# Optimization experiments

Hardware: AMD Instinct MI355X
Metric: run time of the kernel (lower is better)

The kernel has to match this reference:

```python
import jax, jax.numpy as jnp
import numpy as np

B, N, D, S, ITERS, EPS = 32, 4096, 512, 8, 3, 1e-8


def layer_norm(x, g, b, eps=1e-5):
    mu = jnp.mean(x, axis=-1, keepdims=True)
    var = jnp.var(x, axis=-1, keepdims=True)
    return (x - mu) * jax.lax.rsqrt(var + eps) * g + b


def setup_inputs() -> dict:
    key = jax.random.key(0)
    ks = jax.random.split(key, 12)
    sc = 1.0 / np.sqrt(D)
    return {
        "inputs": jax.random.normal(ks[0], (B, N, D), jnp.float32),
        "noise": jax.random.normal(ks[1], (B, S, D), jnp.float32),
        "slots_mu": jax.random.normal(ks[2], (1, S, D), jnp.float32),
        "slots_sigma": jnp.ones((1, S, D), jnp.float32),
        "ln_in_g": jnp.ones((D,), jnp.float32), "ln_in_b": jnp.zeros((D,), jnp.float32),
        "ln_s_g": jnp.ones((D,), jnp.float32), "ln_s_b": jnp.zeros((D,), jnp.float32),
        "wq": jax.random.normal(ks[3], (D, D), jnp.float32) * sc,
        "wk": jax.random.normal(ks[4], (D, D), jnp.float32) * sc,
        "wv": jax.random.normal(ks[5], (D, D), jnp.float32) * sc,
        "w_ih": jax.random.normal(ks[6], (3 * D, D), jnp.float32) * sc,
        "w_hh": jax.random.normal(ks[7], (3 * D, D), jnp.float32) * sc,
        "b_ih": jnp.zeros((3 * D,), jnp.float32),
        "b_hh": jnp.zeros((3 * D,), jnp.float32),
        "ln_m_g": jnp.ones((D,), jnp.float32), "ln_m_b": jnp.zeros((D,), jnp.float32),
        "w1": jax.random.normal(ks[8], (D, D), jnp.float32) * sc,
        "b1": jnp.zeros((D,), jnp.float32),
        "w2": jax.random.normal(ks[9], (D, D), jnp.float32) * sc,
        "b2": jnp.zeros((D,), jnp.float32),
    }


def reference(inputs, noise, slots_mu, slots_sigma, ln_in_g, ln_in_b, ln_s_g, ln_s_b,
              wq, wk, wv, w_ih, w_hh, b_ih, b_hh, ln_m_g, ln_m_b, w1, b1, w2, b2):
    # slot init: mu + sigma * N(0,1)
    slots = slots_mu + slots_sigma * noise          # (B,S,D)
    x = layer_norm(inputs, ln_in_g, ln_in_b)        # (B,N,D)
    k = jnp.einsum('bnd,ed->bne', x, wk)            # (B,N,D)
    v = jnp.einsum('bnd,ed->bne', x, wv)            # (B,N,D)
    for _ in range(ITERS):
        slots_prev = slots
        sn = layer_norm(slots, ln_s_g, ln_s_b)
        q = jnp.einsum('bsd,ed->bse', sn, wq)       # (B,S,D)
        logits = jnp.einsum('bnd,bsd->bns', k, q)   # (B,N,S)
        attn = jax.nn.softmax(logits, axis=-1) + EPS  # softmax over slots
        attn = attn / jnp.sum(attn, axis=-1, keepdims=True)
        attn_t = jnp.swapaxes(attn, -1, -2)         # (B,S,N)
        updates = jnp.einsum('bsn,bnd->bsd', attn_t, v)
        # GRUCell(input=updates, hidden=slots_prev)
        gi = jnp.einsum('bsd,ed->bse', updates, w_ih) + b_ih
        gh = jnp.einsum('bsd,ed->bse', slots_prev, w_hh) + b_hh
        gi_r, gi_z, gi_n = jnp.split(gi, 3, axis=-1)
        gh_r, gh_z, gh_n = jnp.split(gh, 3, axis=-1)
        r = jax.nn.sigmoid(gi_r + gh_r)
        z = jax.nn.sigmoid(gi_z + gh_z)
        n = jnp.tanh(gi_n + r * gh_n)
        slots = (1.0 - z) * n + z * slots_prev
        # residual MLP
        h = layer_norm(slots, ln_m_g, ln_m_b)
        h = jax.nn.relu(jnp.einsum('bsd,ed->bse', h, w1) + b1)
        slots = slots + jnp.einsum('bsd,ed->bse', h, w2) + b2
    return slots
```

## Files before the change

kernel.cpp:

```cpp
#include <hip/hip_runtime.h>

#define B_ 32
#define N_ 4096
#define D_ 512
#define S_ 8
#define ITERS_ 3

__device__ __forceinline__ float sigmoid_f(float x) {
    return 1.0f / (1.0f + __expf(-x));
}
__device__ __forceinline__ float tanh_f(float x) {
    float e = __expf(2.0f * x);
    return 1.0f - 2.0f / (e + 1.0f);
}

__global__ __launch_bounds__(256) void k_init(const float* __restrict__ noise,
                                              const float* __restrict__ mu,
                                              const float* __restrict__ sg,
                                              float* __restrict__ slots,
                                              float* __restrict__ stats) {
    int wid = threadIdx.x >> 6, lane = threadIdx.x & 63;
    int row = blockIdx.x * 4 + wid;
    const float4* nz = (const float4*)(noise + (size_t)row * D_);
    const float4* m4 = (const float4*)(mu + (size_t)(row & 7) * D_);
    const float4* s4 = (const float4*)(sg + (size_t)(row & 7) * D_);
    float4 v0 = nz[lane], v1 = nz[64 + lane];
    float4 a0 = m4[lane], a1 = m4[64 + lane];
    float4 c0 = s4[lane], c1 = s4[64 + lane];
    v0.x = fmaf(c0.x, v0.x, a0.x); v0.y = fmaf(c0.y, v0.y, a0.y);
    v0.z = fmaf(c0.z, v0.z, a0.z); v0.w = fmaf(c0.w, v0.w, a0.w);
    v1.x = fmaf(c1.x, v1.x, a1.x); v1.y = fmaf(c1.y, v1.y, a1.y);
    v1.z = fmaf(c1.z, v1.z, a1.z); v1.w = fmaf(c1.w, v1.w, a1.w);
    float4* o4 = (float4*)(slots + (size_t)row * D_);
    o4[lane] = v0; o4[64 + lane] = v1;
    float s1 = v0.x + v0.y + v0.z + v0.w + v1.x + v1.y + v1.z + v1.w;
    float s2 = v0.x*v0.x; s2 = fmaf(v0.y,v0.y,s2); s2 = fmaf(v0.z,v0.z,s2); s2 = fmaf(v0.w,v0.w,s2);
    s2 = fmaf(v1.x,v1.x,s2); s2 = fmaf(v1.y,v1.y,s2); s2 = fmaf(v1.z,v1.z,s2); s2 = fmaf(v1.w,v1.w,s2);
#pragma unroll
    for (int off = 32; off > 0; off >>= 1) {
        s1 += __shfl_xor(s1, off, 64);
        s2 += __shfl_xor(s2, off, 64);
    }
    if (lane == 0) {
        float mean = s1 * (1.0f / D_);
        float var  = s2 * (1.0f / D_) - mean * mean;
        stats[row * 2]     = mean;
        stats[row * 2 + 1] = rsqrtf(var + 1e-5f);
    }
}

template<int WT, int LNA>
__global__ __launch_bounds__(256) void k_gemm(const float* __restrict__ A,
                                              const float* __restrict__ W,
                                              const float* __restrict__ bias,
                                              float* __restrict__ C,
                                              int M, int N, int K,
                                              const float* __restrict__ stats,
                                              const float* __restrict__ lng,
                                              const float* __restrict__ lnb) {
    __shared__ float As[64][68];
    __shared__ float Ws[64][36];
    int t  = threadIdx.x;
    int bm = blockIdx.y * 64, bn = blockIdx.x * 32;
    int tm = t >> 4, tn = t & 15;
    float acc[4][2] = {{0.f,0.f},{0.f,0.f},{0.f,0.f},{0.f,0.f}};

    for (int kk = 0; kk < K; kk += 64) {
        __syncthreads();
        if (WT == 2) {
#pragma unroll
            for (int r = 0; r < 4; ++r) {
                int idx = t + r * 256;
                int k = idx >> 4, m4 = idx & 15;
                float4 a4 = *(const float4*)(A + (size_t)(kk + k) * M + bm + (m4 << 2));
                *(float4*)&As[k][m4 << 2] = a4;
            }
        } else {
#pragma unroll
            for (int r = 0; r < 4; ++r) {
                int flat = t * 4 + r * 1024;
                int m = flat >> 6, k = flat & 63;
                float4 a4 = *(const float4*)(A + (size_t)(bm + m) * K + kk + k);
                if (LNA) {
                    float mean = stats[(bm + m) * 2];
                    float rs   = stats[(bm + m) * 2 + 1];
                    float4 g4 = *(const float4*)(lng + kk + k);
                    float4 b4 = *(const float4*)(lnb + kk + k);
                    a4.x = fmaf((a4.x - mean) * rs, g4.x, b4.x);
                    a4.y = fmaf((a4.y - mean) * rs, g4.y, b4.y);
                    a4.z = fmaf((a4.z - mean) * rs, g4.z, b4.z);
                    a4.w = fmaf((a4.w - mean) * rs, g4.w, b4.w);
                }
                As[k + 0][m] = a4.x; As[k + 1][m] = a4.y;
                As[k + 2][m] = a4.z; As[k + 3][m] = a4.w;
            }
        }
        if (WT == 1) {
#pragma unroll
            for (int r = 0; r < 2; ++r) {
                int flat = t * 4 + r * 1024;
                int n = flat >> 6, k = flat & 63;
                float4 w4 = *(const float4*)(W + (size_t)(bn + n) * K + kk + k);
                Ws[k + 0][n] = w4.x; Ws[k + 1][n] = w4.y;
                Ws[k + 2][n] = w4.z; Ws[k + 3][n] = w4.w;
            }
        } else {
#pragma unroll
            for (int r = 0; r < 2; ++r) {
                int flat = t * 4 + r * 1024;
                int k = flat >> 5, n = flat & 31;
                float4 w4 = *(const float4*)(W + (size_t)(kk + k) * N + bn + n);
                *(float4*)&Ws[k][n] = w4;
            }
        }
        __syncthreads();
#pragma unroll
        for (int k = 0; k < 64; ++k) {
            float4 a = *(const float4*)&As[k][tm << 2];
            float2 w = *(const float2*)&Ws[k][tn << 1];
            acc[0][0] = fmaf(a.x, w.x, acc[0][0]); acc[0][1] = fmaf(a.x, w.y, acc[0][1]);
            acc[1][0] = fmaf(a.y, w.x, acc[1][0]); acc[1][1] = fmaf(a.y, w.y, acc[1][1]);
            acc[2][0] = fmaf(a.z, w.x, acc[2][0]); acc[2][1] = fmaf(a.z, w.y, acc[2][1]);
            acc[3][0] = fmaf(a.w, w.x, acc[3][0]); acc[3][1] = fmaf(a.w, w.y, acc[3][1]);
        }
    }
#pragma unroll
    for (int i = 0; i < 4; ++i) {
#pragma unroll
        for (int j = 0; j < 2; ++j) {
            int row = bm + (tm << 2) + i;
            int col = bn + (tn << 1) + j;
            float v = acc[i][j];
            if (bias) v += bias[col];
            C[(size_t)row * N + col] = v;
        }
    }
}

__global__ __launch_bounds__(512, 2) void k_attn3(const float* __restrict__ x,
                                                  const float* __restrict__ qk,
                                                  const float* __restrict__ g,
                                                  const float* __restrict__ bvec,
                                                  float* __restrict__ part,
                                                  float* __restrict__ bsum) {
    __shared__ float qts[4096];
    __shared__ float u0s[4096];
    __shared__ float red[64];
    __shared__ float red2[64];
    __shared__ float c12[16];
    const int nc = blockIdx.x, b = blockIdx.y;
    const int t = threadIdx.x;
    const int w = t >> 6, lane = t & 63;

    {
        const float4* qk4 = (const float4*)(qk + (size_t)b * 4096);
        const float4* g4 = (const float4*)g;
        const float4* b4 = (const float4*)bvec;
        float c1p[2], c2p[2];
#pragma unroll
        for (int r = 0; r < 2; ++r) {
            int f = t + r * 512;
            float4 v = qk4[f];
            float4 gg = g4[f & 127];
            float4 bb = b4[f & 127];
            float4 qv = make_float4(v.x*gg.x, v.y*gg.y, v.z*gg.z, v.w*gg.w);
            *(float4*)&qts[((f & 127) * 8 + (f >> 7)) * 4] = qv;
            c1p[r] = qv.x + qv.y + qv.z + qv.w;
            c2p[r] = bb.x*v.x + bb.y*v.y + bb.z*v.z + bb.w*v.w;
        }
#pragma unroll
        for (int off = 32; off > 0; off >>= 1) {
#pragma unroll
            for (int r = 0; r < 2; ++r) {
                c1p[r] += __shfl_xor(c1p[r], off, 64);
                c2p[r] += __shfl_xor(c2p[r], off, 64);
            }
        }
        if (lane == 0) {
            red[w * 2 + 0] = c1p[0]; red[w * 2 + 1] = c1p[1];
            red2[w * 2 + 0] = c2p[0]; red2[w * 2 + 1] = c2p[1];
        }
    }
    __syncthreads();
    if (t < 8) {
        int s = t;
        float v1, v2;
        if (s < 4) { v1 = red[4*s]       + red[4*s + 2];       v2 = red2[4*s]       + red2[4*s + 2]; }
        else       { v1 = red[4*(s-4)+1] + red[4*(s-4)+3];     v2 = red2[4*(s-4)+1] + red2[4*(s-4)+3]; }
        c12[s] = v1; c12[8 + s] = v2;
    }
    __syncthreads();

    float4 qa[8], qb[8];
#pragma unroll
    for (int s = 0; s < 8; ++s) {
        qa[s] = *(const float4*)&qts[(lane * 8 + s) * 4];
        qb[s] = *(const float4*)&qts[((64 + lane) * 8 + s) * 4];
    }
    const int gq = (lane >> 3) & 7;
    const float c1g = c12[gq], c2g = c12[8 + gq];
    const bool hb5 = (lane & 32) != 0, hb4 = (lane & 16) != 0, hb3 = (lane & 8) != 0;
    const int gbase = lane & 7;
    const float cnorm = 1.0f / (1.0f + 8.0f * 1e-8f);
    const float eadd  = 1e-8f * cnorm;

    float4 acc0[8], acc1[8];
#pragma unroll
    for (int s = 0; s < 8; ++s) {
        acc0[s] = make_float4(0.f, 0.f, 0.f, 0.f);
        acc1[s] = make_float4(0.f, 0.f, 0.f, 0.f);
    }
    float aS = 0.f, tS = 0.f;

    const float4* xr = (const float4*)(x + ((size_t)b * N_ + (size_t)nc * 256 + w * 32) * D_);
    float4 xa0 = xr[lane],        xb0 = xr[64 + lane];
    float4 xa1 = xr[128 + lane],  xb1 = xr[192 + lane];

    for (int j = 0; j < 32; ++j) {
        int jn = (j < 30) ? j + 2 : 31;
        float4 na = xr[jn * 128 + lane], nb = xr[jn * 128 + 64 + lane];

        float sx = xa0.x + xa0.y + xa0.z + xa0.w + xb0.x + xb0.y + xb0.z + xb0.w;
        float sxx = xa0.x*xa0.x; sxx = fmaf(xa0.y,xa0.y,sxx); sxx = fmaf(xa0.z,xa0.z,sxx); sxx = fmaf(xa0.w,xa0.w,sxx);
        sxx = fmaf(xb0.x,xb0.x,sxx); sxx = fmaf(xb0.y,xb0.y,sxx); sxx = fmaf(xb0.z,xb0.z,sxx); sxx = fmaf(xb0.w,xb0.w,sxx);
        float dd[8];
#pragma unroll
        for (int s = 0; s < 8; ++s) {
            float td = xa0.x * qa[s].x;
            td = fmaf(xa0.y, qa[s].y, td); td = fmaf(xa0.z, qa[s].z, td); td = fmaf(xa0.w, qa[s].w, td);
            td = fmaf(xb0.x, qb[s].x, td); td = fmaf(xb0.y, qb[s].y, td);
            td = fmaf(xb0.z, qb[s].z, td); td = fmaf(xb0.w, qb[s].w, td);
            dd[s] = td;
        }
        float r4[4];
#pragma unroll
        for (int s = 0; s < 4; ++s) {
            float snd = hb5 ? dd[s] : dd[s + 4];
            float kp  = hb5 ? dd[s + 4] : dd[s];
            r4[s] = kp + __shfl_xor(snd, 32, 64);
        }
        float r2[2];
#pragma unroll
        for (int s = 0; s < 2; ++s) {
            float snd = hb4 ? r4[s] : r4[s + 2];
            float kp  = hb4 ? r4[s + 2] : r4[s];
            r2[s] = kp + __shfl_xor(snd, 16, 64);
        }
        float v;
        {
            float snd = hb3 ? r2[0] : r2[1];
            float kp  = hb3 ? r2[1] : r2[0];
            v = kp + __shfl_xor(snd, 8, 64);
        }
        v += __shfl_xor(v, 4, 64);
        v += __shfl_xor(v, 2, 64);
        v += __shfl_xor(v, 1, 64);
#pragma unroll
        for (int off = 32; off > 0; off >>= 1) {
            sx  += __shfl_xor(sx, off, 64);
            sxx += __shfl_xor(sxx, off, 64);
        }
        float mean = sx * (1.0f / D_);
        float rs   = rsqrtf(sxx * (1.0f / D_) - mean * mean + 1e-5f);
        float lg   = fmaf(rs, v, fmaf(-rs * mean, c1g, c2g));
        float mx = lg;
        mx = fmaxf(mx, __shfl_xor(mx, 8, 64));
        mx = fmaxf(mx, __shfl_xor(mx, 16, 64));
        mx = fmaxf(mx, __shfl_xor(mx, 32, 64));
        float p = __expf(lg - mx);
        float ps = p;
        ps += __shfl_xor(ps, 8, 64);
        ps += __shfl_xor(ps, 16, 64);
        ps += __shfl_xor(ps, 32, 64);
        float a  = fmaf(p, cnorm / ps, eadd);
        float wv = a * rs;
        aS += a;
        tS = fmaf(wv, mean, tS);
        float w8[8];
#pragma unroll
        for (int s = 0; s < 8; ++s) w8[s] = __shfl(wv, (s << 3) | gbase, 64);
#pragma unroll
        for (int s = 0; s < 8; ++s) {
            acc0[s].x = fmaf(w8[s], xa0.x, acc0[s].x); acc0[s].y = fmaf(w8[s], xa0.y, acc0[s].y);
            acc0[s].z = fmaf(w8[s], xa0.z, acc0[s].z); acc0[s].w = fmaf(w8[s], xa0.w, acc0[s].w);
            acc1[s].x = fmaf(w8[s], xb0.x, acc1[s].x); acc1[s].y = fmaf(w8[s], xb0.y, acc1[s].y);
            acc1[s].z = fmaf(w8[s], xb0.z, acc1[s].z); acc1[s].w = fmaf(w8[s], xb0.w, acc1[s].w);
        }
        xa0 = xa1; xb0 = xb1; xa1 = na; xb1 = nb;
    }

    if ((lane & 7) == 0) { red[w * 8 + gq] = aS; red2[w * 8 + gq] = tS; }
    for (int w2 = 0; w2 < 8; ++w2) {
        if (w == w2) {
#pragma unroll
            for (int s = 0; s < 8; ++s) {
                float* p0 = &u0s[s * 512 + (lane << 2)];
                float* p1 = p0 + 256;
                if (w2 == 0) {
                    *(float4*)p0 = acc0[s];
                    *(float4*)p1 = acc1[s];
                } else {
                    float4 v0 = *(float4*)p0;
                    v0.x += acc0[s].x; v0.y += acc0[s].y; v0.z += acc0[s].z; v0.w += acc0[s].w;
                    *(float4*)p0 = v0;
                    float4 v1 = *(float4*)p1;
                    v1.x += acc1[s].x; v1.y += acc1[s].y; v1.z += acc1[s].z; v1.w += acc1[s].w;
                    *(float4*)p1 = v1;
                }
            }
        }
        __syncthreads();
    }
    if (t < 16) {
        int s = t & 7;
        const float* src = (t < 8) ? red : red2;
        float v = 0.f;
#pragma unroll
        for (int w2 = 0; w2 < 8; ++w2) v += src[w2 * 8 + s];
        bsum[(size_t)(b * 16 + nc) * 16 + t] = v;
    }
    float4* d4 = (float4*)(part + (size_t)(b * 16 + nc) * 4096);
    const float4* s4 = (const float4*)u0s;
    d4[t] = s4[t];
    d4[t + 512] = s4[t + 512];
}

__global__ __launch_bounds__(256) void k_ured(const float* __restrict__ part,
                                              const float* __restrict__ bsum,
                                              const float* __restrict__ g,
                                              const float* __restrict__ bvec,
                                              float* __restrict__ u0) {
    __shared__ float avs[16];
    const int b = blockIdx.x, t = threadIdx.x;
    if (t < 16) {
        float v = 0.f;
#pragma unroll
        for (int nc = 0; nc < 16; ++nc) v += bsum[(size_t)(b * 16 + nc) * 16 + t];
        avs[t] = v;
    }
    __syncthreads();
    const int d0 = t * 2;
    float gg0 = g[d0], gg1 = g[d0 + 1], bb0 = bvec[d0], bb1 = bvec[d0 + 1];
#pragma unroll
    for (int s = 0; s < 8; ++s) {
        float p0 = 0.f, p1 = 0.f;
#pragma unroll
        for (int nc = 0; nc < 16; ++nc) {
            float2 pv = *(const float2*)(part + (size_t)(b * 16 + nc) * 4096 + s * 512 + d0);
            p0 += pv.x; p1 += pv.y;
        }
        float Av = avs[s], Tv = avs[8 + s];
        float* o = u0 + (size_t)(b * 8 + s) * D_ + d0;
        o[0] = fmaf(gg0, p0 - Tv, Av * bb0);
        o[1] = fmaf(gg1, p1 - Tv, Av * bb1);
    }
}

__global__ __launch_bounds__(256) void k_gg(const float* __restrict__ slots,
                                            const float* __restrict__ u0,
                                            const float* __restrict__ w_hh,
                                            const float* __restrict__ Wiv,
                                            const float* __restrict__ b_hh,
                                            const float* __restrict__ b_ih,
                                            float* __restrict__ gg) {
    __shared__ float As[64][68];
    __shared__ float Ws[64][36];
    const int t = threadIdx.x;
    const int bx = blockIdx.x;
    const int isGi = (bx >= 48);
    const float* A    = isGi ? u0 : slots;
    const float* W    = isGi ? Wiv : w_hh;
    const float* bias = isGi ? b_ih : b_hh;
    const int bnw = (isGi ? (bx - 48) : bx) * 32;
    const int bnc = bx * 32;
    const int bm  = blockIdx.y * 64;
    int tm = t >> 4, tn = t & 15;
    float acc[4][2] = {{0.f,0.f},{0.f,0.f},{0.f,0.f},{0.f,0.f}};

    for (int kk = 0; kk < 512; kk += 64) {
        __syncthreads();
#pragma unroll
        for (int r = 0; r < 4; ++r) {
            int flat = t * 4 + r * 1024;
            int m = flat >> 6, k = flat & 63;
            float4 a4 = *(const float4*)(A + (size_t)(bm + m) * 512 + kk + k);
            As[k + 0][m] = a4.x; As[k + 1][m] = a4.y;
            As[k + 2][m] = a4.z; As[k + 3][m] = a4.w;
        }
#pragma unroll
        for (int r = 0; r < 2; ++r) {
            int flat = t * 4 + r * 1024;
            int n = flat >> 6, k = flat & 63;
            float4 w4 = *(const float4*)(W + (size_t)(bnw + n) * 512 + kk + k);
            Ws[k + 0][n] = w4.x; Ws[k + 1][n] = w4.y;
            Ws[k + 2][n] = w4.z; Ws[k + 3][n] = w4.w;
        }
        __syncthreads();
#pragma unroll
        for (int k = 0; k < 64; ++k) {
            float4 a = *(const float4*)&As[k][tm << 2];
            float2 w = *(const float2*)&Ws[k][tn << 1];
            acc[0][0] = fmaf(a.x, w.x, acc[0][0]); acc[0][1] = fmaf(a.x, w.y, acc[0][1]);
            acc[1][0] = fmaf(a.y, w.x, acc[1][0]); acc[1][1] = fmaf(a.y, w.y, acc[1][1]);
            acc[2][0] = fmaf(a.z, w.x, acc[2][0]); acc[2][1] = fmaf(a.z, w.y, acc[2][1]);
            acc[3][0] = fmaf(a.w, w.x, acc[3][0]); acc[3][1] = fmaf(a.w, w.y, acc[3][1]);
        }
    }
#pragma unroll
    for (int i = 0; i < 4; ++i) {
#pragma unroll
        for (int j = 0; j < 2; ++j) {
            int row = bm + (tm << 2) + i;
            int cw  = bnw + (tn << 1) + j;
            gg[(size_t)row * 3072 + bnc + (tn << 1) + j] = acc[i][j] + bias[cw];
        }
    }
}

__global__ __launch_bounds__(512) void k_p2(const float* __restrict__ gg,
                                            const float* __restrict__ slots,
                                            const float* __restrict__ w1, const float* __restrict__ b1,
                                            const float* __restrict__ w2, const float* __restrict__ b2,
                                            const float* __restrict__ wqkT,
                                            const float* __restrict__ ln_m_g, const float* __restrict__ ln_m_b,
                                            const float* __restrict__ ln_s_g, const float* __restrict__ ln_s_b,
                                            float* __restrict__ dst, float* __restrict__ qkout, int last) {
    __shared__ float s2s[2][512];
    __shared__ float t0s[2][512];
    __shared__ float hs[2][512];
    __shared__ float stat[4];
    const int t = threadIdx.x;
    const int wid = t >> 6, lane = t & 63;
    const int r0 = blockIdx.x * 2;

#pragma unroll
    for (int j = 0; j < 2; ++j) {
        int flat = t + j * 512;
        int r = flat >> 9, d = flat & 511;
        size_t row = r0 + r;
        const float* ghb = gg + row * 3072;
        const float* gib = ghb + 1536;
        float gir = gib[d], giz = gib[d + 512], gin = gib[d + 1024];
        float ghr = ghb[d], ghz = ghb[d + 512], ghn = ghb[d + 1024];
        float rr = sigmoid_f(gir + ghr);
        float zz = sigmoid_f(giz + ghz);
        float nn = tanh_f(fmaf(rr, ghn, gin));
        float sp = slots[row * 512 + d];
        s2s[r][d] = fmaf(1.0f - zz, nn, zz * sp);
    }
    __syncthreads();
    if (wid < 2) {
        const float4* sr = (const float4*)s2s[wid];
        float4 a = sr[lane], bq = sr[64 + lane];
        float s1 = a.x + a.y + a.z + a.w + bq.x + bq.y + bq.z + bq.w;
        float s2 = a.x*a.x; s2 = fmaf(a.y,a.y,s2); s2 = fmaf(a.z,a.z,s2); s2 = fmaf(a.w,a.w,s2);
        s2 = fmaf(bq.x,bq.x,s2); s2 = fmaf(bq.y,bq.y,s2); s2 = fmaf(bq.z,bq.z,s2); s2 = fmaf(bq.w,bq.w,s2);
#pragma unroll
        for (int off = 32; off > 0; off >>= 1) {
            s1 += __shfl_xor(s1, off, 64);
            s2 += __shfl_xor(s2, off, 64);
        }
        if (lane == 0) {
            float mean = s1 * (1.0f / D_);
            float var  = s2 * (1.0f / D_) - mean * mean;
            stat[wid * 2] = mean;
            stat[wid * 2 + 1] = rsqrtf(var + 1e-5f);
        }
    }
    __syncthreads();
#pragma unroll
    for (int j = 0; j < 2; ++j) {
        int flat = t + j * 512;
        int r = flat >> 9, d = flat & 511;
        t0s[r][d] = fmaf((s2s[r][d] - stat[r * 2]) * stat[r * 2 + 1], ln_m_g[d], ln_m_b[d]);
    }
    __syncthreads();
    {
        const int c = t;
        const float4* wr = (const float4*)(w1 + (size_t)c * 512);
        float a0 = 0.f, a1 = 0.f;
#pragma unroll 8
        for (int k4 = 0; k4 < 128; ++k4) {
            float4 w4 = wr[k4];
            float4 q0 = *(const float4*)&t0s[0][k4 << 2];
            float4 q1 = *(const float4*)&t0s[1][k4 << 2];
            a0 = fmaf(q0.x, w4.x, a0); a0 = fmaf(q0.y, w4.y, a0);
            a0 = fmaf(q0.z, w4.z, a0); a0 = fmaf(q0.w, w4.w, a0);
            a1 = fmaf(q1.x, w4.x, a1); a1 = fmaf(q1.y, w4.y, a1);
            a1 = fmaf(q1.z, w4.z, a1); a1 = fmaf(q1.w, w4.w, a1);
        }
        float bc = b1[c];
        hs[0][c] = fmaxf(a0 + bc, 0.f);
        hs[1][c] = fmaxf(a1 + bc, 0.f);
    }
    __syncthreads();
    {
        const int c = t;
        const float4* wr = (const float4*)(w2 + (size_t)c * 512);
        float a0 = 0.f, a1 = 0.f;
#pragma unroll 8
        for (int k4 = 0; k4 < 128; ++k4) {
            float4 w4 = wr[k4];
            float4 q0 = *(const float4*)&hs[0][k4 << 2];
            float4 q1 = *(const float4*)&hs[1][k4 << 2];
            a0 = fmaf(q0.x, w4.x, a0); a0 = fmaf(q0.y, w4.y, a0);
            a0 = fmaf(q0.z, w4.z, a0); a0 = fmaf(q0.w, w4.w, a0);
            a1 = fmaf(q1.x, w4.x, a1); a1 = fmaf(q1.y, w4.y, a1);
            a1 = fmaf(q1.z, w4.z, a1); a1 = fmaf(q1.w, w4.w, a1);
        }
        float bc = b2[c];
        float o0 = s2s[0][c] + a0 + bc;
        float o1 = s2s[1][c] + a1 + bc;
        dst[(size_t)r0 * 512 + c] = o0;
        dst[(size_t)(r0 + 1) * 512 + c] = o1;
        s2s[0][c] = o0;
        s2s[1][c] = o1;
    }
    if (last) return;
    __syncthreads();
    if (wid < 2) {
        const float4* sr = (const float4*)s2s[wid];
        float4 a = sr[lane], bq = sr[64 + lane];
        float s1 = a.x + a.y + a.z + a.w + bq.x + bq.y + bq.z + bq.w;
        float s2 = a.x*a.x; s2 = fmaf(a.y,a.y,s2); s2 = fmaf(a.z,a.z,s2); s2 = fmaf(a.w,a.w,s2);
        s2 = fmaf(bq.x,bq.x,s2); s2 = fmaf(bq.y,bq.y,s2); s2 = fmaf(bq.z,bq.z,s2); s2 = fmaf(bq.w,bq.w,s2);
#pragma unroll
        for (int off = 32; off > 0; off >>= 1) {
            s1 += __shfl_xor(s1, off, 64);
            s2 += __shfl_xor(s2, off, 64);
        }
        if (lane == 0) {
            float mean = s1 * (1.0f / D_);
            float var  = s2 * (1.0f / D_) - mean * mean;
            stat[wid * 2] = mean;
            stat[wid * 2 + 1] = rsqrtf(var + 1e-5f);
        }
    }
    __syncthreads();
#pragma unroll
    for (int j = 0; j < 2; ++j) {
        int flat = t + j * 512;
        int r = flat >> 9, d = flat & 511;
        t0s[r][d] = fmaf((s2s[r][d] - stat[r * 2]) * stat[r * 2 + 1], ln_s_g[d], ln_s_b[d]);
    }
    __syncthreads();
    {
        const int c = t;
        const float4* wr = (const float4*)(wqkT + (size_t)c * 512);
        float a0 = 0.f, a1 = 0.f;
#pragma unroll 8
        for (int k4 = 0; k4 < 128; ++k4) {
            float4 w4 = wr[k4];
            float4 q0 = *(const float4*)&t0s[0][k4 << 2];
            float4 q1 = *(const float4*)&t0s[1][k4 << 2];
            a0 = fmaf(q0.x, w4.x, a0); a0 = fmaf(q0.y, w4.y, a0);
            a0 = fmaf(q0.z, w4.z, a0); a0 = fmaf(q0.w, w4.w, a0);
            a1 = fmaf(q1.x, w4.x, a1); a1 = fmaf(q1.y, w4.y, a1);
            a1 = fmaf(q1.z, w4.z, a1); a1 = fmaf(q1.w, w4.w, a1);
        }
        qkout[(size_t)r0 * 512 + c] = a0;
        qkout[(size_t)(r0 + 1) * 512 + c] = a1;
    }
}

extern "C" void kernel_launch(void* const* d_in, const int* in_sizes, int n_in,
                              void* d_out, int out_size, void* d_ws, size_t ws_size,
                              hipStream_t stream) {
    const float* inputs  = (const float*)d_in[0];
    const float* noise   = (const float*)d_in[1];
    const float* mu      = (const float*)d_in[2];
    const float* sg      = (const float*)d_in[3];
    const float* ln_in_g = (const float*)d_in[4];
    const float* ln_in_b = (const float*)d_in[5];
    const float* ln_s_g  = (const float*)d_in[6];
    const float* ln_s_b  = (const float*)d_in[7];
    const float* wq      = (const float*)d_in[8];
    const float* wk      = (const float*)d_in[9];
    const float* wv      = (const float*)d_in[10];
    const float* w_ih    = (const float*)d_in[11];
    const float* w_hh    = (const float*)d_in[12];
    const float* b_ih    = (const float*)d_in[13];
    const float* b_hh    = (const float*)d_in[14];
    const float* ln_m_g  = (const float*)d_in[15];
    const float* ln_m_b  = (const float*)d_in[16];
    const float* w1      = (const float*)d_in[17];
    const float* b1      = (const float*)d_in[18];
    const float* w2      = (const float*)d_in[19];
    const float* b2      = (const float*)d_in[20];

    float* ws = (float*)d_ws;
    const size_t SLOT = (size_t)B_ * S_ * D_;
    size_t o = 0;
    float* slots = ws + o; o += SLOT;
    float* qk    = ws + o; o += SLOT;
    float* u0    = ws + o; o += SLOT;
    float* gg    = ws + o; o += (size_t)256 * 3072;
    float* Mqk   = ws + o; o += (size_t)D_ * D_;
    float* Wiv   = ws + o; o += (size_t)3 * D_ * D_;
    float* statsS= ws + o; o += 512;
    float* part  = ws + o; o += (size_t)16 * B_ * 4096;
    float* bsum  = ws + o; o += (size_t)B_ * 16 * 16;

    k_gemm<2,0><<<dim3(16, 8), 256, 0, stream>>>(wk, wq, nullptr, Mqk,
                                                 512, 512, 512, nullptr, nullptr, nullptr);
    k_gemm<0,0><<<dim3(16, 24), 256, 0, stream>>>(w_ih, wv, nullptr, Wiv,
                                                  1536, 512, 512, nullptr, nullptr, nullptr);
    k_init<<<64, 256, 0, stream>>>(noise, mu, sg, slots, statsS);
    k_gemm<1,1><<<dim3(16, 4), 256, 0, stream>>>(slots, Mqk, nullptr, qk,
                                                 256, 512, 512, statsS, ln_s_g, ln_s_b);

    for (int it = 0; it < ITERS_; ++it) {
        k_attn3<<<dim3(16, B_), 512, 0, stream>>>(inputs, qk, ln_in_g, ln_in_b, part, bsum);
        k_ured<<<B_, 256, 0, stream>>>(part, bsum, ln_in_g, ln_in_b, u0);
        k_gg<<<dim3(96, 4), 256, 0, stream>>>(slots, u0, w_hh, Wiv, b_hh, b_ih, gg);
        int last = (it == ITERS_ - 1);
        float* dst = last ? (float*)d_out : slots;
        k_p2<<<128, 512, 0, stream>>>(gg, slots, w1, b1, w2, b2, Mqk,
                                      ln_m_g, ln_m_b, ln_s_g, ln_s_b, dst, qk, last);
    }
}
```

Measured before the change: 730.6 us.

## Fold hidden-state GRU GEMM into attention launch and process token pairs

```diff
diff --git a/kernel.cpp b/kernel.cpp
--- a/kernel.cpp
+++ b/kernel.cpp
@@ -137,19 +137,75 @@
     }
 }
 
-__global__ __launch_bounds__(512, 2) void k_attn3(const float* __restrict__ x,
-                                                  const float* __restrict__ qk,
-                                                  const float* __restrict__ g,
-                                                  const float* __restrict__ bvec,
-                                                  float* __restrict__ part,
-                                                  float* __restrict__ bsum) {
-    __shared__ float qts[4096];
-    __shared__ float u0s[4096];
-    __shared__ float red[64];
-    __shared__ float red2[64];
-    __shared__ float c12[16];
-    const int nc = blockIdx.x, b = blockIdx.y;
+__global__ __launch_bounds__(512, 2) void k_attn_gh(const float* __restrict__ x,
+                                                    const float* __restrict__ qk,
+                                                    const float* __restrict__ g,
+                                                    const float* __restrict__ bvec,
+                                                    float* __restrict__ part,
+                                                    float* __restrict__ bsum,
+                                                    const float* __restrict__ slots,
+                                                    const float* __restrict__ w_hh,
+                                                    const float* __restrict__ b_hh,
+                                                    float* __restrict__ gg) {
+    __shared__ float smem[8704];
+    const int blk = blockIdx.x;
     const int t = threadIdx.x;
+
+    if (blk >= 512) {
+        const int t2 = blk - 512;
+        const int ci = t2 % 24, ri = t2 / 24;
+        const int bm = ri * 64, bn = ci * 64;
+        float (*As)[68] = (float (*)[68])smem;
+        float (*Ws)[68] = (float (*)[68])(smem + 64 * 68);
+        const int tm = t >> 5, tn = t & 31;
+        float acc[4][2] = {{0.f,0.f},{0.f,0.f},{0.f,0.f},{0.f,0.f}};
+        for (int kk = 0; kk < 512; kk += 64) {
+            __syncthreads();
+#pragma unroll
+            for (int r = 0; r < 2; ++r) {
+                int flat = t * 4 + r * 2048;
+                int m = flat >> 6, k = flat & 63;
+                float4 a4 = *(const float4*)(slots + (size_t)(bm + m) * 512 + kk + k);
+                As[k + 0][m] = a4.x; As[k + 1][m] = a4.y;
+                As[k + 2][m] = a4.z; As[k + 3][m] = a4.w;
+            }
+#pragma unroll
+            for (int r = 0; r < 2; ++r) {
+                int flat = t * 4 + r * 2048;
+                int n = flat >> 6, k = flat & 63;
+                float4 w4 = *(const float4*)(w_hh + (size_t)(bn + n) * 512 + kk + k);
+                Ws[k + 0][n] = w4.x; Ws[k + 1][n] = w4.y;
+                Ws[k + 2][n] = w4.z; Ws[k + 3][n] = w4.w;
+            }
+            __syncthreads();
+#pragma unroll
+            for (int k = 0; k < 64; ++k) {
+                const float4 a = *(const float4*)&As[k][tm << 2];
+                const float2 w = *(const float2*)&Ws[k][tn << 1];
+                acc[0][0] = fmaf(a.x, w.x, acc[0][0]); acc[0][1] = fmaf(a.x, w.y, acc[0][1]);
+                acc[1][0] = fmaf(a.y, w.x, acc[1][0]); acc[1][1] = fmaf(a.y, w.y, acc[1][1]);
+                acc[2][0] = fmaf(a.z, w.x, acc[2][0]); acc[2][1] = fmaf(a.z, w.y, acc[2][1]);
+                acc[3][0] = fmaf(a.w, w.x, acc[3][0]); acc[3][1] = fmaf(a.w, w.y, acc[3][1]);
+            }
+        }
+#pragma unroll
+        for (int i = 0; i < 4; ++i) {
+#pragma unroll
+            for (int j = 0; j < 2; ++j) {
+                int row = bm + (tm << 2) + i;
+                int col = bn + (tn << 1) + j;
+                gg[(size_t)row * 3072 + col] = acc[i][j] + b_hh[col];
+            }
+        }
+        return;
+    }
+
+    float* qts  = smem;
+    float* u0s  = smem + 4096;
+    float* red  = smem + 8192;
+    float* red2 = smem + 8256;
+    float* c12  = smem + 8320;
+    const int nc = blk & 15, b = blk >> 4;
     const int w = t >> 6, lane = t & 63;
 
     {
@@ -161,9 +217,9 @@
         for (int r = 0; r < 2; ++r) {
             int f = t + r * 512;
             float4 v = qk4[f];
-            float4 gg = g4[f & 127];
+            float4 gg4 = g4[f & 127];
             float4 bb = b4[f & 127];
-            float4 qv = make_float4(v.x*gg.x, v.y*gg.y, v.z*gg.z, v.w*gg.w);
+            float4 qv = make_float4(v.x*gg4.x, v.y*gg4.y, v.z*gg4.z, v.w*gg4.w);
             *(float4*)&qts[((f & 127) * 8 + (f >> 7)) * 4] = qv;
             c1p[r] = qv.x + qv.y + qv.z + qv.w;
             c2p[r] = bb.x*v.x + bb.y*v.y + bb.z*v.z + bb.w*v.w;
@@ -213,81 +269,126 @@
     float aS = 0.f, tS = 0.f;
 
     const float4* xr = (const float4*)(x + ((size_t)b * N_ + (size_t)nc * 256 + w * 32) * D_);
-    float4 xa0 = xr[lane],        xb0 = xr[64 + lane];
-    float4 xa1 = xr[128 + lane],  xb1 = xr[192 + lane];
-
-    for (int j = 0; j < 32; ++j) {
-        int jn = (j < 30) ? j + 2 : 31;
-        float4 na = xr[jn * 128 + lane], nb = xr[jn * 128 + 64 + lane];
-
-        float sx = xa0.x + xa0.y + xa0.z + xa0.w + xb0.x + xb0.y + xb0.z + xb0.w;
-        float sxx = xa0.x*xa0.x; sxx = fmaf(xa0.y,xa0.y,sxx); sxx = fmaf(xa0.z,xa0.z,sxx); sxx = fmaf(xa0.w,xa0.w,sxx);
-        sxx = fmaf(xb0.x,xb0.x,sxx); sxx = fmaf(xb0.y,xb0.y,sxx); sxx = fmaf(xb0.z,xb0.z,sxx); sxx = fmaf(xb0.w,xb0.w,sxx);
-        float dd[8];
+    float4 cur0 = xr[lane],       cur1 = xr[64 + lane];
+    float4 cur2 = xr[128 + lane], cur3 = xr[192 + lane];
+
+#define DOTS(X0, X1, R)                                                          \
+    {                                                                            \
+        sx[R] = (X0).x + (X0).y + (X0).z + (X0).w                                \
+              + (X1).x + (X1).y + (X1).z + (X1).w;                               \
+        float t_ = (X0).x*(X0).x;                                                \
+        t_ = fmaf((X0).y,(X0).y,t_); t_ = fmaf((X0).z,(X0).z,t_);                \
+        t_ = fmaf((X0).w,(X0).w,t_); t_ = fmaf((X1).x,(X1).x,t_);                \
+        t_ = fmaf((X1).y,(X1).y,t_); t_ = fmaf((X1).z,(X1).z,t_);                \
+        t_ = fmaf((X1).w,(X1).w,t_); sxx[R] = t_;                                \
+        _Pragma("unroll")                                                        \
+        for (int s = 0; s < 8; ++s) {                                            \
+            float td = (X0).x * qa[s].x;                                         \
+            td = fmaf((X0).y, qa[s].y, td); td = fmaf((X0).z, qa[s].z, td);      \
+            td = fmaf((X0).w, qa[s].w, td);                                      \
+            td = fmaf((X1).x, qb[s].x, td); td = fmaf((X1).y, qb[s].y, td);      \
+            td = fmaf((X1).z, qb[s].z, td); td = fmaf((X1).w, qb[s].w, td);      \
+            dd[R][s] = td;                                                       \
+        }                                                                        \
+    }
+
+    for (int jp = 0; jp < 16; ++jp) {
+        int jn = (jp < 15) ? (2 * jp + 2) : 30;
+        float4 n0 = xr[jn * 128 + lane],       n1 = xr[jn * 128 + 64 + lane];
+        float4 n2 = xr[(jn + 1) * 128 + lane], n3 = xr[(jn + 1) * 128 + 64 + lane];
+
+        float sx[2], sxx[2], dd[2][8];
+        DOTS(cur0, cur1, 0);
+        DOTS(cur2, cur3, 1);
+
+        float r4[2][4];
+#pragma unroll
+        for (int r = 0; r < 2; ++r) {
+#pragma unroll
+            for (int s = 0; s < 4; ++s) {
+                float snd = hb5 ? dd[r][s] : dd[r][s + 4];
+                float kp  = hb5 ? dd[r][s + 4] : dd[r][s];
+                r4[r][s] = kp + __shfl_xor(snd, 32, 64);
+            }
+        }
+        float r2v[2][2];
+#pragma unroll
+        for (int r = 0; r < 2; ++r) {
+#pragma unroll
+            for (int s = 0; s < 2; ++s) {
+                float snd = hb4 ? r4[r][s] : r4[r][s + 2];
+                float kp  = hb4 ? r4[r][s + 2] : r4[r][s];
+                r2v[r][s] = kp + __shfl_xor(snd, 16, 64);
+            }
+        }
+        float vv[2];
+#pragma unroll
+        for (int r = 0; r < 2; ++r) {
+            float snd = hb3 ? r2v[r][0] : r2v[r][1];
+            float kp  = hb3 ? r2v[r][1] : r2v[r][0];
+            vv[r] = kp + __shfl_xor(snd, 8, 64);
+        }
+#pragma unroll
+        for (int off = 4; off > 0; off >>= 1) {
+#pragma unroll
+            for (int r = 0; r < 2; ++r) vv[r] += __shfl_xor(vv[r], off, 64);
+        }
+#pragma unroll
+        for (int off = 32; off > 0; off >>= 1) {
+#pragma unroll
+            for (int r = 0; r < 2; ++r) {
+                sx[r]  += __shfl_xor(sx[r], off, 64);
+                sxx[r] += __shfl_xor(sxx[r], off, 64);
+            }
+        }
+        float mean[2], rsv[2], lg[2];
+#pragma unroll
+        for (int r = 0; r < 2; ++r) {
+            mean[r] = sx[r] * (1.0f / D_);
+            rsv[r]  = rsqrtf(sxx[r] * (1.0f / D_) - mean[r] * mean[r] + 1e-5f);
+            lg[r]   = fmaf(rsv[r], vv[r], fmaf(-rsv[r] * mean[r], c1g, c2g));
+        }
+        float mx[2] = { lg[0], lg[1] };
+#pragma unroll
+        for (int r = 0; r < 2; ++r) {
+            mx[r] = fmaxf(mx[r], __shfl_xor(mx[r], 8, 64));
+            mx[r] = fmaxf(mx[r], __shfl_xor(mx[r], 16, 64));
+            mx[r] = fmaxf(mx[r], __shfl_xor(mx[r], 32, 64));
+        }
+        float pv[2], ps[2];
+#pragma unroll
+        for (int r = 0; r < 2; ++r) { pv[r] = __expf(lg[r] - mx[r]); ps[r] = pv[r]; }
+#pragma unroll
+        for (int r = 0; r < 2; ++r) {
+            ps[r] += __shfl_xor(ps[r], 8, 64);
+            ps[r] += __shfl_xor(ps[r], 16, 64);
+            ps[r] += __shfl_xor(ps[r], 32, 64);
+        }
+        float av[2], wv[2];
+#pragma unroll
+        for (int r = 0; r < 2; ++r) {
+            av[r] = fmaf(pv[r], cnorm / ps[r], eadd);
+            wv[r] = av[r] * rsv[r];
+        }
+        aS += av[0]; aS += av[1];
+        tS = fmaf(wv[0], mean[0], tS);
+        tS = fmaf(wv[1], mean[1], tS);
 #pragma unroll
         for (int s = 0; s < 8; ++s) {
-            float td = xa0.x * qa[s].x;
-            td = fmaf(xa0.y, qa[s].y, td); td = fmaf(xa0.z, qa[s].z, td); td = fmaf(xa0.w, qa[s].w, td);
-            td = fmaf(xb0.x, qb[s].x, td); td = fmaf(xb0.y, qb[s].y, td);
-            td = fmaf(xb0.z, qb[s].z, td); td = fmaf(xb0.w, qb[s].w, td);
-            dd[s] = td;
-        }
-        float r4[4];
-#pragma unroll
-        for (int s = 0; s < 4; ++s) {
-            float snd = hb5 ? dd[s] : dd[s + 4];
-            float kp  = hb5 ? dd[s + 4] : dd[s];
-            r4[s] = kp + __shfl_xor(snd, 32, 64);
-        }
-        float r2[2];
-#pragma unroll
-        for (int s = 0; s < 2; ++s) {
-            float snd = hb4 ? r4[s] : r4[s + 2];
-            float kp  = hb4 ? r4[s + 2] : r4[s];
-            r2[s] = kp + __shfl_xor(snd, 16, 64);
-        }
-        float v;
-        {
-            float snd = hb3 ? r2[0] : r2[1];
-            float kp  = hb3 ? r2[1] : r2[0];
-            v = kp + __shfl_xor(snd, 8, 64);
-        }
-        v += __shfl_xor(v, 4, 64);
-        v += __shfl_xor(v, 2, 64);
-        v += __shfl_xor(v, 1, 64);
-#pragma unroll
-        for (int off = 32; off > 0; off >>= 1) {
-            sx  += __shfl_xor(sx, off, 64);
-            sxx += __shfl_xor(sxx, off, 64);
-        }
-        float mean = sx * (1.0f / D_);
-        float rs   = rsqrtf(sxx * (1.0f / D_) - mean * mean + 1e-5f);
-        float lg   = fmaf(rs, v, fmaf(-rs * mean, c1g, c2g));
-        float mx = lg;
-        mx = fmaxf(mx, __shfl_xor(mx, 8, 64));
-        mx = fmaxf(mx, __shfl_xor(mx, 16, 64));
-        mx = fmaxf(mx, __shfl_xor(mx, 32, 64));
-        float p = __expf(lg - mx);
-        float ps = p;
-        ps += __shfl_xor(ps, 8, 64);
-        ps += __shfl_xor(ps, 16, 64);
-        ps += __shfl_xor(ps, 32, 64);
-        float a  = fmaf(p, cnorm / ps, eadd);
-        float wv = a * rs;
-        aS += a;
-        tS = fmaf(wv, mean, tS);
-        float w8[8];
-#pragma unroll
-        for (int s = 0; s < 8; ++s) w8[s] = __shfl(wv, (s << 3) | gbase, 64);
-#pragma unroll
-        for (int s = 0; s < 8; ++s) {
-            acc0[s].x = fmaf(w8[s], xa0.x, acc0[s].x); acc0[s].y = fmaf(w8[s], xa0.y, acc0[s].y);
-            acc0[s].z = fmaf(w8[s], xa0.z, acc0[s].z); acc0[s].w = fmaf(w8[s], xa0.w, acc0[s].w);
-            acc1[s].x = fmaf(w8[s], xb0.x, acc1[s].x); acc1[s].y = fmaf(w8[s], xb0.y, acc1[s].y);
-            acc1[s].z = fmaf(w8[s], xb0.z, acc1[s].z); acc1[s].w = fmaf(w8[s], xb0.w, acc1[s].w);
-        }
-        xa0 = xa1; xb0 = xb1; xa1 = na; xb1 = nb;
-    }
+            float w0 = __shfl(wv[0], (s << 3) | gbase, 64);
+            float w1 = __shfl(wv[1], (s << 3) | gbase, 64);
+            acc0[s].x = fmaf(w0, cur0.x, acc0[s].x); acc0[s].y = fmaf(w0, cur0.y, acc0[s].y);
+            acc0[s].z = fmaf(w0, cur0.z, acc0[s].z); acc0[s].w = fmaf(w0, cur0.w, acc0[s].w);
+            acc1[s].x = fmaf(w0, cur1.x, acc1[s].x); acc1[s].y = fmaf(w0, cur1.y, acc1[s].y);
+            acc1[s].z = fmaf(w0, cur1.z, acc1[s].z); acc1[s].w = fmaf(w0, cur1.w, acc1[s].w);
+            acc0[s].x = fmaf(w1, cur2.x, acc0[s].x); acc0[s].y = fmaf(w1, cur2.y, acc0[s].y);
+            acc0[s].z = fmaf(w1, cur2.z, acc0[s].z); acc0[s].w = fmaf(w1, cur2.w, acc0[s].w);
+            acc1[s].x = fmaf(w1, cur3.x, acc1[s].x); acc1[s].y = fmaf(w1, cur3.y, acc1[s].y);
+            acc1[s].z = fmaf(w1, cur3.z, acc1[s].z); acc1[s].w = fmaf(w1, cur3.w, acc1[s].w);
+        }
+        cur0 = n0; cur1 = n1; cur2 = n2; cur3 = n3;
+    }
+#undef DOTS
 
     if ((lane & 7) == 0) { red[w * 8 + gq] = aS; red2[w * 8 + gq] = tS; }
     for (int w2 = 0; w2 < 8; ++w2) {
@@ -325,55 +426,36 @@
     d4[t + 512] = s4[t + 512];
 }
 
-__global__ __launch_bounds__(256) void k_ured(const float* __restrict__ part,
+__global__ __launch_bounds__(512) void k_ured(const float* __restrict__ part,
                                               const float* __restrict__ bsum,
                                               const float* __restrict__ g,
                                               const float* __restrict__ bvec,
                                               float* __restrict__ u0) {
-    __shared__ float avs[16];
-    const int b = blockIdx.x, t = threadIdx.x;
-    if (t < 16) {
-        float v = 0.f;
-#pragma unroll
-        for (int nc = 0; nc < 16; ++nc) v += bsum[(size_t)(b * 16 + nc) * 16 + t];
-        avs[t] = v;
-    }
-    __syncthreads();
-    const int d0 = t * 2;
-    float gg0 = g[d0], gg1 = g[d0 + 1], bb0 = bvec[d0], bb1 = bvec[d0 + 1];
-#pragma unroll
-    for (int s = 0; s < 8; ++s) {
-        float p0 = 0.f, p1 = 0.f;
-#pragma unroll
-        for (int nc = 0; nc < 16; ++nc) {
-            float2 pv = *(const float2*)(part + (size_t)(b * 16 + nc) * 4096 + s * 512 + d0);
-            p0 += pv.x; p1 += pv.y;
-        }
-        float Av = avs[s], Tv = avs[8 + s];
-        float* o = u0 + (size_t)(b * 8 + s) * D_ + d0;
-        o[0] = fmaf(gg0, p0 - Tv, Av * bb0);
-        o[1] = fmaf(gg1, p1 - Tv, Av * bb1);
-    }
-}
-
-__global__ __launch_bounds__(256) void k_gg(const float* __restrict__ slots,
-                                            const float* __restrict__ u0,
-                                            const float* __restrict__ w_hh,
+    const int bs = blockIdx.x;
+    const int b = bs >> 3, s = bs & 7;
+    const int d = threadIdx.x;
+    float Av = 0.f, Tv = 0.f;
+#pragma unroll
+    for (int nc = 0; nc < 16; ++nc) {
+        Av += bsum[(size_t)(b * 16 + nc) * 16 + s];
+        Tv += bsum[(size_t)(b * 16 + nc) * 16 + 8 + s];
+    }
+    float p = 0.f;
+#pragma unroll
+    for (int nc = 0; nc < 16; ++nc)
+        p += part[(size_t)(b * 16 + nc) * 4096 + s * 512 + d];
+    u0[(size_t)bs * 512 + d] = fmaf(g[d], p - Tv, Av * bvec[d]);
+}
+
+__global__ __launch_bounds__(256) void k_gi(const float* __restrict__ u0,
                                             const float* __restrict__ Wiv,
-                                            const float* __restrict__ b_hh,
                                             const float* __restrict__ b_ih,
                                             float* __restrict__ gg) {
     __shared__ float As[64][68];
     __shared__ float Ws[64][36];
     const int t = threadIdx.x;
-    const int bx = blockIdx.x;
-    const int isGi = (bx >= 48);
-    const float* A    = isGi ? u0 : slots;
-    const float* W    = isGi ? Wiv : w_hh;
-    const float* bias = isGi ? b_ih : b_hh;
-    const int bnw = (isGi ? (bx - 48) : bx) * 32;
-    const int bnc = bx * 32;
-    const int bm  = blockIdx.y * 64;
+    const int bn = blockIdx.x * 32;
+    const int bm = blockIdx.y * 64;
     int tm = t >> 4, tn = t & 15;
     float acc[4][2] = {{0.f,0.f},{0.f,0.f},{0.f,0.f},{0.f,0.f}};
 
@@ -383,7 +465,7 @@
         for (int r = 0; r < 4; ++r) {
             int flat = t * 4 + r * 1024;
             int m = flat >> 6, k = flat & 63;
-            float4 a4 = *(const float4*)(A + (size_t)(bm + m) * 512 + kk + k);
+            float4 a4 = *(const float4*)(u0 + (size_t)(bm + m) * 512 + kk + k);
             As[k + 0][m] = a4.x; As[k + 1][m] = a4.y;
             As[k + 2][m] = a4.z; As[k + 3][m] = a4.w;
         }
@@ -391,7 +473,7 @@
         for (int r = 0; r < 2; ++r) {
             int flat = t * 4 + r * 1024;
             int n = flat >> 6, k = flat & 63;
-            float4 w4 = *(const float4*)(W + (size_t)(bnw + n) * 512 + kk + k);
+            float4 w4 = *(const float4*)(Wiv + (size_t)(bn + n) * 512 + kk + k);
             Ws[k + 0][n] = w4.x; Ws[k + 1][n] = w4.y;
             Ws[k + 2][n] = w4.z; Ws[k + 3][n] = w4.w;
         }
@@ -411,8 +493,8 @@
 #pragma unroll
         for (int j = 0; j < 2; ++j) {
             int row = bm + (tm << 2) + i;
-            int cw  = bnw + (tn << 1) + j;
-            gg[(size_t)row * 3072 + bnc + (tn << 1) + j] = acc[i][j] + bias[cw];
+            int cw  = bn + (tn << 1) + j;
+            gg[(size_t)row * 3072 + 1536 + cw] = acc[i][j] + b_ih[cw];
         }
     }
 }
@@ -610,9 +692,10 @@
                                                  256, 512, 512, statsS, ln_s_g, ln_s_b);
 
     for (int it = 0; it < ITERS_; ++it) {
-        k_attn3<<<dim3(16, B_), 512, 0, stream>>>(inputs, qk, ln_in_g, ln_in_b, part, bsum);
-        k_ured<<<B_, 256, 0, stream>>>(part, bsum, ln_in_g, ln_in_b, u0);
-        k_gg<<<dim3(96, 4), 256, 0, stream>>>(slots, u0, w_hh, Wiv, b_hh, b_ih, gg);
+        k_attn_gh<<<608, 512, 0, stream>>>(inputs, qk, ln_in_g, ln_in_b, part, bsum,
+                                           slots, w_hh, b_hh, gg);
+        k_ured<<<256, 512, 0, stream>>>(part, bsum, ln_in_g, ln_in_b, u0);
+        k_gi<<<dim3(48, 4), 256, 0, stream>>>(u0, Wiv, b_ih, gg);
         int last = (it == ITERS_ - 1);
         float* dst = last ? (float*)d_out : slots;
         k_p2<<<128, 512, 0, stream>>>(gg, slots, w1, b1, w2, b2, Mqk,
```

Result: faster. 700.4 us (-4.1%).
